# Performance work log

Hardware: AMD Instinct MI355X
Metric: run time of the kernel (lower is better)

## Reference

```python
import jax, jax.numpy as jnp
import numpy as np

N, E, D_EDGE, C, H, W, HID = 10000, 160000, 64, 16, 8, 8, 128


def setup_inputs() -> dict:
    key = jax.random.key(0)
    ks = jax.random.split(key, 7)
    x = jax.random.normal(ks[0], (N, C, H, W), jnp.float32)
    edge_attr = jax.random.normal(ks[1], (E, D_EDGE), jnp.float32)
    edge_index = jax.random.randint(ks[2], (2, E), 0, N, dtype=jnp.int64)
    W1 = jax.random.normal(ks[3], (D_EDGE, HID), jnp.float32) * 0.1
    b1 = jnp.zeros((HID,), jnp.float32)
    W2 = jax.random.normal(ks[4], (HID, 1), jnp.float32) * 0.1
    b2 = jnp.zeros((1,), jnp.float32)
    Wn = jax.random.normal(ks[5], (C, 3 * C), jnp.float32) * 0.1
    bn = jnp.zeros((C,), jnp.float32)
    return dict(x=x, edge_attr=edge_attr, W1=W1, b1=b1, W2=W2, b2=b2,
                Wn=Wn, bn=bn, edge_index=edge_index)


def _masked_scatter_softmax(logits, seg, mask, n):
    # softmax over edges grouped by seg, restricted to mask==True edges.
    # Masked edges get -inf logits -> exp 0 -> zero weight (same math as
    # boolean-indexing the edge subset in the torch original).
    neg = jnp.where(mask[:, None], logits, -jnp.inf)          # [E, 1]
    m = jax.ops.segment_max(neg, seg, num_segments=n)         # [N, 1]
    m = jnp.where(jnp.isfinite(m), m, 0.0)                    # empty segments
    e = jnp.exp(neg - m[seg])                                 # [E, 1], 0 where masked
    s = jax.ops.segment_sum(e, seg, num_segments=n)           # [N, 1]
    return e / jnp.maximum(s[seg], 1e-30)


def _flow(x, logits, row, col, mask, n):
    w = _masked_scatter_softmax(logits, row, mask, n)         # [E, 1]
    msg = x[col] * w[:, :, None, None]                        # [E, C, H, W]
    return jax.ops.segment_sum(msg, row, num_segments=n)      # [N, C, H, W]


def reference(x, edge_attr, W1, b1, W2, b2, Wn, bn, edge_index):
    row, col = edge_index[0], edge_index[1]
    # cls_net: MLP edge classifier producing per-edge logit [E, 1]
    h = jax.nn.relu(edge_attr @ W1 + b1)
    dec_edge_feats = h @ W2 + b2
    n = x.shape[0]
    flow_out = _flow(x, dec_edge_feats, row, col, row < col, n)
    flow_in = _flow(x, dec_edge_feats, row, col, row > col, n)
    flow = jnp.concatenate([x, flow_in, flow_out], axis=1)    # [N, 3C, H, W]
    # node_model: 1x1 conv over channels
    out = jnp.einsum('nchw,oc->nohw', flow, Wn) + bn[None, :, None, None]
    return out, dec_edge_feats
```

## Files before the change

### kernel.cpp

```cpp
#include <hip/hip_runtime.h>

#define N_NODES 10000
#define N_EDGES 160000
#define D_EDGE  64
#define C_CH    16
#define HW      64
#define HID     128
#define NODE_ELEMS 1024
#define NSEG    (2 * N_NODES)
#define CAP     64
#define MLPB    625
#define QUANTB  625
#define XPITCH  72

typedef __attribute__((ext_vector_type(8))) short short8;
typedef __attribute__((ext_vector_type(4))) float f32x4;

__device__ __forceinline__ unsigned bf16_rne(float f) {
    unsigned u = __float_as_uint(f);
    return (u + 0x7FFFu + ((u >> 16) & 1u)) >> 16;
}
__device__ __forceinline__ short8 pack_bf16x8(float4 lo, float4 hi) {
    union { unsigned u[4]; short8 s; } r;
    r.u[0] = bf16_rne(lo.x) | (bf16_rne(lo.y) << 16);
    r.u[1] = bf16_rne(lo.z) | (bf16_rne(lo.w) << 16);
    r.u[2] = bf16_rne(hi.x) | (bf16_rne(hi.y) << 16);
    r.u[3] = bf16_rne(hi.z) | (bf16_rne(hi.w) << 16);
    return r.s;
}

__global__ __launch_bounds__(256) void k_prep(
    const float* __restrict__ W1, const float* __restrict__ Wn,
    unsigned short* __restrict__ W1bfT, unsigned short* __restrict__ WnTb,
    unsigned* __restrict__ zbase)
{
    int tid = threadIdx.x;
    if (blockIdx.x < 4) {
        int q  = blockIdx.x * 256 + tid;
        int n  = q >> 3;
        int ko = (q & 7) * 8;
        #pragma unroll
        for (int i = 0; i < 8; ++i) {
            int k = ko + i;
            W1bfT[n * 64 + k] = (unsigned short)bf16_rne(W1[k * HID + n]);
        }
    } else if (blockIdx.x == 4) {
        int q = tid * 4;
        int o = q >> 6, k0 = q & 63;
        #pragma unroll
        for (int i = 0; i < 4; ++i) {
            int k = k0 + i;
            WnTb[o * 64 + k] =
                (k < 48) ? (unsigned short)bf16_rne(Wn[o * 48 + k]) : 0;
        }
    } else {
        int idx = (blockIdx.x - 5) * 256 + tid;
        for (int i = idx; i < NSEG; i += 64 * 256) zbase[i] = 0u;
    }
}

__device__ __forceinline__ unsigned pb4(float4 f, float inv) {
    int a = (int)rintf(f.x * inv) + 128;
    int b = (int)rintf(f.y * inv) + 128;
    int c = (int)rintf(f.z * inv) + 128;
    int d = (int)rintf(f.w * inv) + 128;
    a = min(255, max(0, a)); b = min(255, max(0, b));
    c = min(255, max(0, c)); d = min(255, max(0, d));
    return (unsigned)a | ((unsigned)b << 8) | ((unsigned)c << 16) | ((unsigned)d << 24);
}
__global__ __launch_bounds__(256) void k_mlpcast(
    const float* __restrict__ ea, const unsigned short* __restrict__ W1bfT,
    const float* __restrict__ b1, const float* __restrict__ W2,
    const float* __restrict__ b2,
    const int* __restrict__ row, const int* __restrict__ col,
    const float* __restrict__ x, unsigned char* __restrict__ xq,
    float* __restrict__ scale,
    float* __restrict__ dec,
    int* __restrict__ cursor, int2* __restrict__ bucket)
{
    const int tid  = threadIdx.x;
    const int lane = tid & 63, wv = tid >> 6;

    if (blockIdx.x >= MLPB) {
        const int nb = (blockIdx.x - MLPB) * 16 + wv * 4;
        const int ln = lane;
        float4 v[2][4];
        {
            const float4* xs = (const float4*)(x + (size_t)nb * NODE_ELEMS) + ln * 4;
            v[0][0] = xs[0]; v[0][1] = xs[1]; v[0][2] = xs[2]; v[0][3] = xs[3];
        }
        #pragma unroll
        for (int j = 0; j < 4; ++j) {
            if (j < 3) {
                const float4* xs =
                    (const float4*)(x + (size_t)(nb + j + 1) * NODE_ELEMS) + ln * 4;
                v[(j + 1) & 1][0] = xs[0]; v[(j + 1) & 1][1] = xs[1];
                v[(j + 1) & 1][2] = xs[2]; v[(j + 1) & 1][3] = xs[3];
            }
            float4 v0 = v[j & 1][0], v1 = v[j & 1][1];
            float4 v2 = v[j & 1][2], v3 = v[j & 1][3];
            float m = fmaxf(fmaxf(fmaxf(fabsf(v0.x), fabsf(v0.y)),
                                  fmaxf(fabsf(v0.z), fabsf(v0.w))),
                     fmaxf(fmaxf(fmaxf(fabsf(v1.x), fabsf(v1.y)),
                                  fmaxf(fabsf(v1.z), fabsf(v1.w))),
                     fmaxf(fmaxf(fmaxf(fabsf(v2.x), fabsf(v2.y)),
                                  fmaxf(fabsf(v2.z), fabsf(v2.w))),
                           fmaxf(fmaxf(fabsf(v3.x), fabsf(v3.y)),
                                  fmaxf(fabsf(v3.z), fabsf(v3.w))))));
            #pragma unroll
            for (int off = 1; off < 64; off <<= 1)
                m = fmaxf(m, __shfl_xor(m, off));
            m = fmaxf(m, 1e-20f);
            float inv = 127.0f / m;
            uint4 o;
            o.x = pb4(v0, inv); o.y = pb4(v1, inv);
            o.z = pb4(v2, inv); o.w = pb4(v3, inv);
            ((uint4*)(xq + (size_t)(nb + j) * NODE_ELEMS))[ln] = o;
            if (ln == 0) scale[nb + j] = m * (1.0f / 127.0f);
        }
        return;
    }

    const int i15 = lane & 15, g = lane >> 4;
    const int ebase = blockIdx.x * 256 + wv * 64;

    int e_c[4], seg[4], pos[4];
    if (lane < 16) {
        #pragma unroll
        for (int t = 0; t < 4; ++t) {
            int e = ebase + t * 16 + lane;
            int r = row[e], c = col[e];
            e_c[t] = c; pos[t] = -1; seg[t] = 0;
            if (r != c) {
                seg[t] = 2 * r + ((r < c) ? 0 : 1);
                pos[t] = atomicAdd(&cursor[seg[t]], 1);
            }
        }
    }

    float w2v[8], bv[8];
    #pragma unroll
    for (int t8 = 0; t8 < 8; ++t8) {
        w2v[t8] = W2[t8 * 16 + i15];
        bv[t8]  = b1[t8 * 16 + i15];
    }
    const float b2v = b2[0];

    short8 bfrag[2][8];
    #pragma unroll
    for (int kt = 0; kt < 2; ++kt)
        #pragma unroll
        for (int t8 = 0; t8 < 8; ++t8)
            bfrag[kt][t8] =
                *(const short8*)&W1bfT[(t8 * 16 + i15) * 64 + kt * 32 + g * 8];

    short8 aF[2][2];
    #pragma unroll
    for (int kt = 0; kt < 2; ++kt) {
        const float4* src =
            (const float4*)&ea[(size_t)(ebase + i15) * D_EDGE + kt * 32 + g * 8];
        aF[0][kt] = pack_bf16x8(src[0], src[1]);
    }

    #pragma unroll
    for (int t = 0; t < 4; ++t) {
        if (t < 3) {
            #pragma unroll
            for (int kt = 0; kt < 2; ++kt) {
                const float4* src = (const float4*)
                    &ea[(size_t)(ebase + (t + 1) * 16 + i15) * D_EDGE + kt * 32 + g * 8];
                aF[(t + 1) & 1][kt] = pack_bf16x8(src[0], src[1]);
            }
        }
        f32x4 acc[8];
        #pragma unroll
        for (int t8 = 0; t8 < 8; ++t8) acc[t8] = (f32x4){0.f, 0.f, 0.f, 0.f};
        #pragma unroll
        for (int kt = 0; kt < 2; ++kt)
            #pragma unroll
            for (int t8 = 0; t8 < 8; ++t8)
                acc[t8] = __builtin_amdgcn_mfma_f32_16x16x32_bf16(
                    aF[t & 1][kt], bfrag[kt][t8], acc[t8], 0, 0, 0);

        float loc[4] = {0.f, 0.f, 0.f, 0.f};
        #pragma unroll
        for (int t8 = 0; t8 < 8; ++t8) {
            #pragma unroll
            for (int r = 0; r < 4; ++r)
                loc[r] = fmaf(fmaxf(acc[t8][r] + bv[t8], 0.f), w2v[t8], loc[r]);
        }
        #pragma unroll
        for (int r = 0; r < 4; ++r) {
            #pragma unroll
            for (int off = 1; off < 16; off <<= 1)
                loc[r] += __shfl_xor(loc[r], off);
        }
        int srcl = ((lane & 15) >> 2) << 4;
        float t0 = __shfl(loc[0], srcl), t1 = __shfl(loc[1], srcl);
        float t2 = __shfl(loc[2], srcl), t3 = __shfl(loc[3], srcl);
        if (lane < 16) {
            int rr = lane & 3;
            float logit = ((rr == 0) ? t0 : (rr == 1) ? t1 : (rr == 2) ? t2 : t3)
                          + b2v;
            dec[ebase + t * 16 + lane] = logit;
            if (pos[t] >= 0 && pos[t] < CAP) {
                float ex = expf(logit);
                bucket[((size_t)seg[t] << 6) + pos[t]] =
                    make_int2(e_c[t], __float_as_int(ex));
            }
        }
    }
}

__device__ __forceinline__ void acc8(float* A, uint2 v, float ws) {
    A[0] = fmaf(ws, (float)( v.x        & 255u), A[0]);
    A[1] = fmaf(ws, (float)((v.x >>  8) & 255u), A[1]);
    A[2] = fmaf(ws, (float)((v.x >> 16) & 255u), A[2]);
    A[3] = fmaf(ws, (float)( v.x >> 24        ), A[3]);
    A[4] = fmaf(ws, (float)( v.y        & 255u), A[4]);
    A[5] = fmaf(ws, (float)((v.y >>  8) & 255u), A[5]);
    A[6] = fmaf(ws, (float)((v.y >> 16) & 255u), A[6]);
    A[7] = fmaf(ws, (float)( v.y >> 24        ), A[7]);
}

__global__ __launch_bounds__(128) void k_gather(
    const float* __restrict__ x, const unsigned char* __restrict__ xq,
    const float* __restrict__ scale,
    const int* __restrict__ cursor, const int2* __restrict__ bucket,
    const unsigned short* __restrict__ WnTb, const float* __restrict__ bn,
    float* __restrict__ out)
{
    const int n = blockIdx.x;
    const int t = threadIdx.x;

    __shared__ __align__(16) unsigned short sxf[64 * XPITCH];
    __shared__ int2  s_ecw[2 * CAP];
    __shared__ float s_ex[2 * CAP];

    {
        int zr = t >> 1, zk = 48 + (t & 1) * 8;
        *(uint4*)&sxf[zr * XPITCH + zk] = make_uint4(0, 0, 0, 0);
    }

    const int c0  = min(cursor[2 * n],     CAP);
    const int c1  = min(cursor[2 * n + 1], CAP);
    const int tot = c0 + c1;
    if (t < tot) {
        int2 e = (t < c0) ? bucket[((size_t)(2 * n) << 6) + t]
                          : bucket[((size_t)(2 * n + 1) << 6) + t - c0];
        float ex = __int_as_float(e.y);
        s_ex[t] = ex;
        e.y = __float_as_int(ex * scale[e.x]);
        s_ecw[t] = e;
    }
    __syncthreads();

    float sum0 = 0.f, sum1 = 0.f;
    for (int i = 0; i < c0; ++i)   sum0 += s_ex[i];
    for (int i = c0; i < tot; ++i) sum1 += s_ex[i];

    float a[8] = {0,0,0,0,0,0,0,0};
    float b[8] = {0,0,0,0,0,0,0,0};
    float wsA = 0.f, wsB = 0.f;
    const uint2* xqt = (const uint2*)xq + t;

#define FMAJ(J) { float ws = __int_as_float(s_ecw[i + (J)].y);                \
                  if (i + (J) < c0) { acc8(a, v[J], ws); wsA += ws; }         \
                  else              { acc8(b, v[J], ws); wsB += ws; } }

    int i = 0;
    for (; i + 16 <= tot; i += 16) {
        uint2 v[16];
        #pragma unroll
        for (int j = 0; j < 16; ++j) v[j] = xqt[(size_t)s_ecw[i + j].x * 128];
        #pragma unroll
        for (int j = 0; j < 16; ++j) FMAJ(j)
    }
    for (; i + 8 <= tot; i += 8) {
        uint2 v[8];
        #pragma unroll
        for (int j = 0; j < 8; ++j) v[j] = xqt[(size_t)s_ecw[i + j].x * 128];
        #pragma unroll
        for (int j = 0; j < 8; ++j) FMAJ(j)
    }
    for (; i + 4 <= tot; i += 4) {
        uint2 v[4];
        #pragma unroll
        for (int j = 0; j < 4; ++j) v[j] = xqt[(size_t)s_ecw[i + j].x * 128];
        #pragma unroll
        for (int j = 0; j < 4; ++j) FMAJ(j)
    }
    for (; i < tot; ++i) {
        uint2 v[1];
        v[0] = xqt[(size_t)s_ecw[i].x * 128];
        FMAJ(0)
    }
#undef FMAJ

    const int c_of_t = t >> 3, hw0 = (t & 7) * 8;
    const float4* xsrc = (const float4*)(x + (size_t)n * NODE_ELEMS) + t * 2;
    float4 xv0 = xsrc[0], xv1 = xsrc[1];

    const float r0 = 1.0f / fmaxf(sum0, 1e-30f);
    const float r1 = 1.0f / fmaxf(sum1, 1e-30f);
    const float o0 = 128.0f * wsA, o1 = 128.0f * wsB;
    float xv[8] = {xv0.x, xv0.y, xv0.z, xv0.w, xv1.x, xv1.y, xv1.z, xv1.w};
    #pragma unroll
    for (int j = 0; j < 8; ++j) {
        unsigned short* rowp = &sxf[(hw0 + j) * XPITCH];
        rowp[     c_of_t] = (unsigned short)bf16_rne(xv[j]);
        rowp[16 + c_of_t] = (unsigned short)bf16_rne((b[j] - o1) * r1);
        rowp[32 + c_of_t] = (unsigned short)bf16_rne((a[j] - o0) * r0);
    }
    __syncthreads();

    const int lane = t & 63, wv = t >> 6;
    const int i15 = lane & 15, g = lane >> 4;
    const float bno = bn[i15];
    float* outb = out + (size_t)n * NODE_ELEMS;

    #pragma unroll
    for (int mt = 0; mt < 2; ++mt) {
        const int mrow = (wv * 2 + mt) * 16;
        f32x4 accm = (f32x4){bno, bno, bno, bno};
        #pragma unroll
        for (int kt = 0; kt < 2; ++kt) {
            short8 af = *(const short8*)&sxf[(mrow + i15) * XPITCH + kt * 32 + g * 8];
            short8 bf = *(const short8*)&WnTb[i15 * 64 + kt * 32 + g * 8];
            accm = __builtin_amdgcn_mfma_f32_16x16x32_bf16(af, bf, accm, 0, 0, 0);
        }
        const int hwb = mrow + g * 4;
        #pragma unroll
        for (int r = 0; r < 4; ++r)
            outb[i15 * 64 + hwb + r] = accm[r];
    }
}

extern "C" void kernel_launch(void* const* d_in, const int* in_sizes, int n_in,
                              void* d_out, int out_size, void* d_ws, size_t ws_size,
                              hipStream_t stream)
{
    const float* x         = (const float*)d_in[0];
    const float* edge_attr = (const float*)d_in[1];
    const float* W1        = (const float*)d_in[2];
    const float* b1        = (const float*)d_in[3];
    const float* W2        = (const float*)d_in[4];
    const float* b2        = (const float*)d_in[5];
    const float* Wn        = (const float*)d_in[6];
    const float* bn        = (const float*)d_in[7];
    const int*   eidx      = (const int*)d_in[8];
    const int*   row       = eidx;
    const int*   col       = eidx + N_EDGES;

    float* out = (float*)d_out;
    float* dec = out + (size_t)N_NODES * NODE_ELEMS;

    unsigned char* xq     = (unsigned char*)d_ws;
    float*         scale  = (float*)(xq + (size_t)N_NODES * NODE_ELEMS);
    int2*          bucket = (int2*)(scale + N_NODES);
    int*           cursor = (int*)(bucket + (size_t)NSEG * CAP);
    unsigned short* W1bfT = (unsigned short*)(cursor + NSEG);
    unsigned short* WnTb  = W1bfT + D_EDGE * HID;

    k_prep<<<69, 256, 0, stream>>>(W1, Wn, W1bfT, WnTb, (unsigned*)cursor);
    k_mlpcast<<<MLPB + QUANTB, 256, 0, stream>>>(edge_attr, W1bfT, b1, W2, b2,
                                                 row, col, x, xq, scale,
                                                 dec, cursor, bucket);
    k_gather<<<N_NODES, 128, 0, stream>>>(x, xq, scale, cursor,
                                          bucket, WnTb, bn, out);
}
```

Before: 75.38 us.

## Store quantized x channel-last and XOR-swizzle the gather LDS tile

The quantize pass now writes each node's int8 copy transposed, as [hw][channel], so each gather thread owns eight consecutive channels of one spatial position. That lets k_gather pack x, flow_in and flow_out into three 16-byte bf16 stores per thread instead of 24 scalar 2-byte LDS stores. The padded LDS pitch is replaced by an XOR swizzle on 8-element groups to avoid bank conflicts for both the stores and the MFMA A-operand reads. The cost is that the x reads in both kernels change from float4 vector loads to strided scalar loads, which are still coalesced across lanes.

```diff
diff --git a/kernel.cpp b/kernel.cpp
--- a/kernel.cpp
+++ b/kernel.cpp
@@ -11,7 +11,6 @@
 #define CAP     64
 #define MLPB    625
 #define QUANTB  625
-#define XPITCH  72
 
 typedef __attribute__((ext_vector_type(8))) short short8;
 typedef __attribute__((ext_vector_type(4))) float f32x4;
@@ -27,6 +26,14 @@
     r.u[2] = bf16_rne(hi.x) | (bf16_rne(hi.y) << 16);
     r.u[3] = bf16_rne(hi.z) | (bf16_rne(hi.w) << 16);
     return r.s;
+}
+__device__ __forceinline__ uint4 pkbf8(const float* v) {
+    uint4 o;
+    o.x = bf16_rne(v[0]) | (bf16_rne(v[1]) << 16);
+    o.y = bf16_rne(v[2]) | (bf16_rne(v[3]) << 16);
+    o.z = bf16_rne(v[4]) | (bf16_rne(v[5]) << 16);
+    o.w = bf16_rne(v[6]) | (bf16_rne(v[7]) << 16);
+    return o;
 }
 
 __global__ __launch_bounds__(256) void k_prep(
@@ -59,11 +66,11 @@
     }
 }
 
-__device__ __forceinline__ unsigned pb4(float4 f, float inv) {
-    int a = (int)rintf(f.x * inv) + 128;
-    int b = (int)rintf(f.y * inv) + 128;
-    int c = (int)rintf(f.z * inv) + 128;
-    int d = (int)rintf(f.w * inv) + 128;
+__device__ __forceinline__ unsigned pb4a(const float* v, float inv) {
+    int a = (int)rintf(v[0] * inv) + 128;
+    int b = (int)rintf(v[1] * inv) + 128;
+    int c = (int)rintf(v[2] * inv) + 128;
+    int d = (int)rintf(v[3] * inv) + 128;
     a = min(255, max(0, a)); b = min(255, max(0, b));
     c = min(255, max(0, c)); d = min(255, max(0, d));
     return (unsigned)a | ((unsigned)b << 8) | ((unsigned)c << 16) | ((unsigned)d << 24);
@@ -84,37 +91,30 @@
     if (blockIdx.x >= MLPB) {
         const int nb = (blockIdx.x - MLPB) * 16 + wv * 4;
         const int ln = lane;
-        float4 v[2][4];
-        {
-            const float4* xs = (const float4*)(x + (size_t)nb * NODE_ELEMS) + ln * 4;
-            v[0][0] = xs[0]; v[0][1] = xs[1]; v[0][2] = xs[2]; v[0][3] = xs[3];
-        }
+        float v[2][16];
+        #pragma unroll
+        for (int c = 0; c < 16; ++c)
+            v[0][c] = x[(size_t)nb * NODE_ELEMS + c * HW + ln];
         #pragma unroll
         for (int j = 0; j < 4; ++j) {
             if (j < 3) {
-                const float4* xs =
-                    (const float4*)(x + (size_t)(nb + j + 1) * NODE_ELEMS) + ln * 4;
-                v[(j + 1) & 1][0] = xs[0]; v[(j + 1) & 1][1] = xs[1];
-                v[(j + 1) & 1][2] = xs[2]; v[(j + 1) & 1][3] = xs[3];
+                #pragma unroll
+                for (int c = 0; c < 16; ++c)
+                    v[(j + 1) & 1][c] =
+                        x[(size_t)(nb + j + 1) * NODE_ELEMS + c * HW + ln];
             }
-            float4 v0 = v[j & 1][0], v1 = v[j & 1][1];
-            float4 v2 = v[j & 1][2], v3 = v[j & 1][3];
-            float m = fmaxf(fmaxf(fmaxf(fabsf(v0.x), fabsf(v0.y)),
-                                  fmaxf(fabsf(v0.z), fabsf(v0.w))),
-                     fmaxf(fmaxf(fmaxf(fabsf(v1.x), fabsf(v1.y)),
-                                  fmaxf(fabsf(v1.z), fabsf(v1.w))),
-                     fmaxf(fmaxf(fmaxf(fabsf(v2.x), fabsf(v2.y)),
-                                  fmaxf(fabsf(v2.z), fabsf(v2.w))),
-                           fmaxf(fmaxf(fabsf(v3.x), fabsf(v3.y)),
-                                  fmaxf(fabsf(v3.z), fabsf(v3.w))))));
+            const float* vj = v[j & 1];
+            float m = 0.f;
+            #pragma unroll
+            for (int c = 0; c < 16; ++c) m = fmaxf(m, fabsf(vj[c]));
             #pragma unroll
             for (int off = 1; off < 64; off <<= 1)
                 m = fmaxf(m, __shfl_xor(m, off));
             m = fmaxf(m, 1e-20f);
             float inv = 127.0f / m;
             uint4 o;
-            o.x = pb4(v0, inv); o.y = pb4(v1, inv);
-            o.z = pb4(v2, inv); o.w = pb4(v3, inv);
+            o.x = pb4a(vj +  0, inv); o.y = pb4a(vj +  4, inv);
+            o.z = pb4a(vj +  8, inv); o.w = pb4a(vj + 12, inv);
             ((uint4*)(xq + (size_t)(nb + j) * NODE_ELEMS))[ln] = o;
             if (ln == 0) scale[nb + j] = m * (1.0f / 127.0f);
         }
@@ -233,13 +233,14 @@
     const int n = blockIdx.x;
     const int t = threadIdx.x;
 
-    __shared__ __align__(16) unsigned short sxf[64 * XPITCH];
+    __shared__ __align__(16) unsigned short sxf[64 * 64];
     __shared__ int2  s_ecw[2 * CAP];
     __shared__ float s_ex[2 * CAP];
 
     {
-        int zr = t >> 1, zk = 48 + (t & 1) * 8;
-        *(uint4*)&sxf[zr * XPITCH + zk] = make_uint4(0, 0, 0, 0);
+        int zr = t >> 1;
+        int zg = (6 + (t & 1)) ^ (zr & 7);
+        *(uint4*)&sxf[zr * 64 + zg * 8] = make_uint4(0, 0, 0, 0);
     }
 
     const int c0  = min(cursor[2 * n],     CAP);
@@ -297,20 +298,27 @@
     }
 #undef FMAJ
 
-    const int c_of_t = t >> 3, hw0 = (t & 7) * 8;
-    const float4* xsrc = (const float4*)(x + (size_t)n * NODE_ELEMS) + t * 2;
-    float4 xv0 = xsrc[0], xv1 = xsrc[1];
+    const int hw = t >> 1, c8 = (t & 1) * 8;
+    float xv[8];
+    #pragma unroll
+    for (int j = 0; j < 8; ++j)
+        xv[j] = x[(size_t)n * NODE_ELEMS + (c8 + j) * HW + hw];
 
     const float r0 = 1.0f / fmaxf(sum0, 1e-30f);
     const float r1 = 1.0f / fmaxf(sum1, 1e-30f);
     const float o0 = 128.0f * wsA, o1 = 128.0f * wsB;
-    float xv[8] = {xv0.x, xv0.y, xv0.z, xv0.w, xv1.x, xv1.y, xv1.z, xv1.w};
+    float fin[8], fout[8];
     #pragma unroll
     for (int j = 0; j < 8; ++j) {
-        unsigned short* rowp = &sxf[(hw0 + j) * XPITCH];
-        rowp[     c_of_t] = (unsigned short)bf16_rne(xv[j]);
-        rowp[16 + c_of_t] = (unsigned short)bf16_rne((b[j] - o1) * r1);
-        rowp[32 + c_of_t] = (unsigned short)bf16_rne((a[j] - o0) * r0);
+        fout[j] = (a[j] - o0) * r0;
+        fin[j]  = (b[j] - o1) * r1;
+    }
+    {
+        unsigned short* rowp = &sxf[hw * 64];
+        const int swz = hw & 7, half = t & 1;
+        *(uint4*)&rowp[((0 + half) ^ swz) * 8] = pkbf8(xv);
+        *(uint4*)&rowp[((2 + half) ^ swz) * 8] = pkbf8(fin);
+        *(uint4*)&rowp[((4 + half) ^ swz) * 8] = pkbf8(fout);
     }
     __syncthreads();
 
@@ -325,7 +333,9 @@
         f32x4 accm = (f32x4){bno, bno, bno, bno};
         #pragma unroll
         for (int kt = 0; kt < 2; ++kt) {
-            short8 af = *(const short8*)&sxf[(mrow + i15) * XPITCH + kt * 32 + g * 8];
+            const int r = mrow + i15;
+            const int gk = (kt * 4 + g) ^ (r & 7);
+            short8 af = *(const short8*)&sxf[r * 64 + gk * 8];
             short8 bf = *(const short8*)&WnTb[i15 * 64 + kt * 32 + g * 8];
             accm = __builtin_amdgcn_mfma_f32_16x16x32_bf16(af, bf, accm, 0, 0, 0);
         }
```

After: 74.28 us, median of 2. No clear change (-1.5%).
